# Performance work log

Hardware: AMD Instinct MI355X
Metric: run time of the kernel (lower is better)

The kernel has to match this reference:

```python
import jax, jax.numpy as jnp
import numpy as np

NUM_QUBITS = 12
NUM_LAYERS = 2
STATE_DIM = 2 ** NUM_QUBITS
BATCH = 4096
TWO_PI = 2 * 3.1416  # matches the original initializer constant


def _u3(theta, phi, lam):
    """Single-qubit U3 gate, 2x2 complex64 (matches TF layer exactly)."""
    c = jnp.cos(theta / 2)
    s = jnp.sin(theta / 2)
    z = jnp.zeros_like(phi)
    e_phi = jnp.exp(jax.lax.complex(z, phi))
    e_lam = jnp.exp(jax.lax.complex(z, lam))
    e_pl = jnp.exp(jax.lax.complex(z, phi + lam))
    cc = jax.lax.complex(c, jnp.zeros_like(c))
    sc = jax.lax.complex(s, jnp.zeros_like(s))
    row1 = jnp.stack([cc, -e_lam * sc])
    row2 = jnp.stack([e_phi * sc, e_pl * cc])
    return jnp.stack([row1, row2])  # [2, 2] complex64


def _full_gate(theta_vec, phi_vec, lam_vec):
    """Kronecker product of per-qubit gates -> [2^n, 2^n] complex64."""
    full = _u3(theta_vec[0], phi_vec[0], lam_vec[0])
    for q in range(1, theta_vec.shape[0]):
        full = jnp.kron(full, _u3(theta_vec[q], phi_vec[q], lam_vec[q]))
    return full


def setup_inputs() -> dict:
    key = jax.random.key(0)
    k1, k2, k3, k4 = jax.random.split(key, 4)
    inputs = jax.random.normal(k1, (BATCH, STATE_DIM), dtype=jnp.float32)
    thetas = jax.random.uniform(k2, (NUM_LAYERS, NUM_QUBITS), minval=0.0, maxval=TWO_PI, dtype=jnp.float32)
    phis = jax.random.uniform(k3, (NUM_LAYERS, NUM_QUBITS), minval=0.0, maxval=TWO_PI, dtype=jnp.float32)
    lams = jax.random.uniform(k4, (NUM_LAYERS, NUM_QUBITS), minval=0.0, maxval=TWO_PI, dtype=jnp.float32)
    return {"inputs": inputs, "thetas": thetas, "phis": phis, "lams": lams}


def reference(inputs, thetas, phis, lams):
    # normalize real inputs as complex state, per-sample L2 norm
    state = jax.lax.complex(inputs, jnp.zeros_like(inputs))  # [B, D] complex64
    norm = jnp.linalg.norm(state, axis=1, keepdims=True)      # real, [B, 1]
    state = state / norm
    for l in range(thetas.shape[0]):
        U = _full_gate(thetas[l], phis[l], lams[l])  # [D, D]
        # matvec(U, x) per sample == state @ U^T, batched GEMM replaces tf.map_fn
        state = state @ U.T
    return jnp.real(state * jnp.conj(state))  # probabilities, [B, D] float32
```

## Files before the change

### kernel.cpp

```cpp
#include <hip/hip_runtime.h>
#include <hip/hip_fp16.h>

#define NQ   12
#define DIM  4096
#define NL   2
#define BATCH 4096

typedef float  v2f __attribute__((ext_vector_type(2)));
typedef __fp16 hv2 __attribute__((ext_vector_type(2)));


struct HGate { __half2 m[8]; };

__global__ void build_gates(const float* __restrict__ th,
                            const float* __restrict__ ph,
                            const float* __restrict__ lm,
                            float* __restrict__ gates) {
    int q = threadIdx.x;
    if (q >= NQ) return;
    float g00r = 1.f, g00i = 0.f, g01r = 0.f, g01i = 0.f;
    float g10r = 0.f, g10i = 0.f, g11r = 1.f, g11i = 0.f;
    #pragma unroll
    for (int l = 0; l < NL; ++l) {
        float th2 = 0.5f * th[l * NQ + q];
        float p   = ph[l * NQ + q];
        float la  = lm[l * NQ + q];
        float s, c, sl, cl, sp, cp, spl, cpl;
        sincosf(th2, &s, &c);
        sincosf(la, &sl, &cl);
        sincosf(p, &sp, &cp);
        sincosf(p + la, &spl, &cpl);
        float u00r = c,        u00i = 0.f;
        float u01r = -cl * s,  u01i = -sl * s;
        float u10r = cp * s,   u10i = sp * s;
        float u11r = cpl * c,  u11i = spl * c;
        float n00r = u00r*g00r - u00i*g00i + u01r*g10r - u01i*g10i;
        float n00i = u00r*g00i + u00i*g00r + u01r*g10i + u01i*g10r;
        float n01r = u00r*g01r - u00i*g01i + u01r*g11r - u01i*g11i;
        float n01i = u00r*g01i + u00i*g01r + u01r*g11i + u01i*g11r;
        float n10r = u10r*g00r - u10i*g00i + u11r*g10r - u11i*g10i;
        float n10i = u10r*g00i + u10i*g00r + u11r*g10i + u11i*g10r;
        float n11r = u10r*g01r - u10i*g01i + u11r*g11r - u11i*g11i;
        float n11i = u10r*g01i + u10i*g01r + u11r*g11i + u11i*g11r;
        g00r = n00r; g00i = n00i; g01r = n01r; g01i = n01i;
        g10r = n10r; g10i = n10i; g11r = n11r; g11i = n11i;
    }
    int k = (NQ - 1) - q;
    __half2* o = reinterpret_cast<__half2*>(gates) + (size_t)k * 8;
    o[0] = __floats2half2_rn(g00r,  g00i);
    o[1] = __floats2half2_rn(-g00i, g00i);
    o[2] = __floats2half2_rn(g01r,  g01i);
    o[3] = __floats2half2_rn(-g01i, g01i);
    o[4] = __floats2half2_rn(g10r,  g10i);
    o[5] = __floats2half2_rn(-g10i, g10i);
    o[6] = __floats2half2_rn(g11r,  g11i);
    o[7] = __floats2half2_rn(-g11i, g11i);
}

__device__ __forceinline__ unsigned h2u(__half2 x) {
    union { __half2 h; unsigned u; } c; c.h = x; return c.u;
}
__device__ __forceinline__ __half2 u2h(unsigned x) {
    union { unsigned u; __half2 h; } c; c.u = x; return c.h;
}
__device__ __forceinline__ __half2 rbroad(float x) {
    union { hv2 a; __half2 b; } c;
    c.a = __builtin_amdgcn_cvt_pkrtz(x, x);
    return c.b;
}

__device__ __forceinline__ __half2 cfma(__half2 g1, __half2 g2, __half2 x,
                                        __half2 acc) {
    acc = __hfma2(__low2half2(g1), x, acc);
    acc = __hfma2(g2, __lowhigh2highlow(x), acc);
    return acc;
}

__device__ __forceinline__ void papply(__half2 v[16], int r0, int r1,
                                       const HGate& g) {
    __half2 x0 = v[r0], x1 = v[r1];
    __half2 a = __hmul2(__low2half2(g.m[2]), x1);
    a = __hfma2(g.m[3], __lowhigh2highlow(x1), a);
    a = cfma(g.m[0], g.m[1], x0, a);
    __half2 b = __hmul2(__low2half2(g.m[6]), x1);
    b = __hfma2(g.m[7], __lowhigh2highlow(x1), b);
    b = cfma(g.m[4], g.m[5], x0, b);
    v[r0] = a; v[r1] = b;
}

__device__ __forceinline__ void papply_rbit(__half2 v[16], int rb,
                                            const HGate& g) {
    const int m = 1 << rb;
    #pragma unroll
    for (int h = 0; h < 8; ++h) {
        int low = h & (m - 1);
        int r   = ((h & ~(m - 1)) << 1) | low;
        papply(v, r, r | m, g);
    }
}

#define K1W(r) ( (((r)&1)*33) + ((((r)>>1)&1)*66) + ((((r)>>2)&1)*264) + ((((r)>>3)&1)*512) )
#define K1R(r) (r)
#define K2W(r) ( ((((r)&1))<<2) | (((((r)>>1)&1))<<3) | (((((r)>>2)&1))<<4) | (((((r)>>3)&1))<<8) )
#define K3R(r) ( (((r)&1)*36) + ((((r)>>1)&1)*72) + ((((r)>>2)&1)*1024) + ((((r)>>3)&1)*2048) )

__global__ __launch_bounds__(256, 8)
void qc_sim(const float* __restrict__ in,
            const HGate* __restrict__ gp,
            float* __restrict__ out) {
    __shared__ unsigned st[DIM];
    __shared__ float red[4];

    const int t    = threadIdx.x;
    const int lane = t & 63;
    const int b    = blockIdx.x;

    const float4* __restrict__ x4 =
        reinterpret_cast<const float4*>(in + (size_t)b * DIM);
    float4 lA[4];
    #pragma unroll
    for (int j = 0; j < 4; ++j) lA[j] = x4[j * 256 + t];

    float ss = 0.f;
    #pragma unroll
    for (int j = 0; j < 4; ++j)
        ss += lA[j].x*lA[j].x + lA[j].y*lA[j].y + lA[j].z*lA[j].z + lA[j].w*lA[j].w;
    #pragma unroll
    for (int off = 32; off > 0; off >>= 1)
        ss += __shfl_down(ss, off, 64);
    if (lane == 0) red[t >> 6] = ss;

    const int L0 = lane & 1, L1 = (lane >> 1) & 1, L2 = (lane >> 2) & 1,
              L3 = (lane >> 3) & 1, L4 = (lane >> 4) & 1, L5 = lane >> 5;
    const int w  = t >> 6, w0 = w & 1, w1 = w >> 1;
    const int A1w = L0 | (L1 << 1) | ((L2 ^ L5) << 2) | (L3 << 3) | (L4 << 4)
                  | (L5 << 7) | (w << 10);
    const int A1r = L0 | (L1 << 1) | (L3 << 2) | (L4 << 3) | (L2 << 4)
                  | (L0 << 5) | (L1 << 6) | (L3 << 7) | (L4 << 8) | (L5 << 9)
                  | (w << 10);
    const int A2w = L0 | (L1 << 1) | (L2 << 2) | (L3 << 3) | (L4 << 4)
                  | (L2 << 5) | (L3 << 6) | (L4 << 7) | (L5 << 9) | (w << 10);
    const int A3  = L0 | (L1 << 1) | (L2 << 2) | (L3 << 3) | ((L4 ^ w0) << 4)
                  | (w0 << 7) | (L5 << 8) | (w1 << 9);

    __half2 v[16];

    {
        HGate g0 = gp[0];
        #pragma unroll
        for (int j = 0; j < 4; ++j) {
            __half2 xx0 = rbroad(lA[j].x), xx1 = rbroad(lA[j].y);
            v[4*j]   = __hfma2(g0.m[2], xx1, __hmul2(g0.m[0], xx0));
            v[4*j+1] = __hfma2(g0.m[6], xx1, __hmul2(g0.m[4], xx0));
            xx0 = rbroad(lA[j].z); xx1 = rbroad(lA[j].w);
            v[4*j+2] = __hfma2(g0.m[2], xx1, __hmul2(g0.m[0], xx0));
            v[4*j+3] = __hfma2(g0.m[6], xx1, __hmul2(g0.m[4], xx0));
        }
        { HGate g = gp[1];  papply_rbit(v, 1, g); }
        { HGate g = gp[10]; papply_rbit(v, 2, g); }
        { HGate g = gp[11];
          #pragma unroll
          for (int h = 0; h < 8; ++h) {
              papply(v, h, h | 8, g);
              st[A1w ^ K1W(h)]     = h2u(v[h]);
              st[A1w ^ K1W(h | 8)] = h2u(v[h | 8]);
          }
        }
    }

    #pragma unroll
    for (int r = 0; r < 16; ++r) v[r] = u2h(st[A1r ^ K1R(r)]);

    { HGate g = gp[2]; papply_rbit(v, 0, g); }
    { HGate g = gp[3]; papply_rbit(v, 1, g); }
    { HGate g = gp[4]; papply_rbit(v, 2, g); }
    { HGate g = gp[5];
      #pragma unroll
      for (int h = 0; h < 8; ++h) {
          papply(v, h, h | 8, g);
          st[A2w ^ K2W(h)]     = h2u(v[h]);
          st[A2w ^ K2W(h | 8)] = h2u(v[h | 8]);
      }
    }

    __syncthreads();

    #pragma unroll
    for (int r = 0; r < 16; ++r) v[r] = u2h(st[A3 ^ K3R(r)]);

    { HGate g = gp[6]; papply_rbit(v, 0, g); }
    { HGate g = gp[7]; papply_rbit(v, 1, g); }
    { HGate g = gp[8]; papply_rbit(v, 2, g); }
    { HGate g = gp[9]; papply_rbit(v, 3, g); }

    float inv = 1.0f / (red[0] + red[1] + red[2] + red[3]);
    const int sbase = lane | (w << 10);
    float* __restrict__ o = out + (size_t)b * DIM;
    #pragma unroll
    for (int r = 0; r < 16; ++r) {
        float re = __low2float(v[r]), im = __high2float(v[r]);
        o[sbase + (r << 6)] = (re * re + im * im) * inv;
    }
}

extern "C" void kernel_launch(void* const* d_in, const int* in_sizes, int n_in,
                              void* d_out, int out_size, void* d_ws, size_t ws_size,
                              hipStream_t stream) {
    (void)in_sizes; (void)n_in; (void)out_size; (void)ws_size;
    const float* inputs = (const float*)d_in[0];
    const float* thetas = (const float*)d_in[1];
    const float* phis   = (const float*)d_in[2];
    const float* lams   = (const float*)d_in[3];
    float* gates = (float*)d_ws;
    float* out   = (float*)d_out;

    hipLaunchKernelGGL(build_gates, dim3(1), dim3(64), 0, stream,
                       thetas, phis, lams, gates);
    hipLaunchKernelGGL(qc_sim, dim3(BATCH), dim3(256), 0, stream,
                       inputs, (const HGate*)gates, out);
}
```

Baseline: 128.4 us.

## Process two batch samples per block with packed 64-bit LDS exchanges

Each block now simulates two samples at once. Their half2 amplitudes are packed into 64-bit words for the shared-memory transposes, and the grid is halved. This amortizes gate loads, index math and syncs across two states and uses wider LDS accesses, with new swizzle constants for the 8-byte layout. In exchange it doubles register and LDS use per block, and occupancy is lowered via launch bounds (256,4).

After: 128.1 us. No clear change (-0.2%).

```diff
diff --git a/kernel.cpp b/kernel.cpp
--- a/kernel.cpp
+++ b/kernel.cpp
@@ -69,137 +69,163 @@
     return c.b;
 }
 
-__device__ __forceinline__ __half2 cfma(__half2 g1, __half2 g2, __half2 x,
-                                        __half2 acc) {
-    acc = __hfma2(__low2half2(g1), x, acc);
-    acc = __hfma2(g2, __lowhigh2highlow(x), acc);
-    return acc;
-}
-
-__device__ __forceinline__ void papply(__half2 v[16], int r0, int r1,
-                                       const HGate& g) {
-    __half2 x0 = v[r0], x1 = v[r1];
+__device__ __forceinline__ void cbfly(__half2& x0, __half2& x1, const HGate& g) {
     __half2 a = __hmul2(__low2half2(g.m[2]), x1);
     a = __hfma2(g.m[3], __lowhigh2highlow(x1), a);
-    a = cfma(g.m[0], g.m[1], x0, a);
+    a = __hfma2(__low2half2(g.m[0]), x0, a);
+    a = __hfma2(g.m[1], __lowhigh2highlow(x0), a);
     __half2 b = __hmul2(__low2half2(g.m[6]), x1);
     b = __hfma2(g.m[7], __lowhigh2highlow(x1), b);
-    b = cfma(g.m[4], g.m[5], x0, b);
-    v[r0] = a; v[r1] = b;
-}
-
-__device__ __forceinline__ void papply_rbit(__half2 v[16], int rb,
-                                            const HGate& g) {
+    b = __hfma2(__low2half2(g.m[4]), x0, b);
+    b = __hfma2(g.m[5], __lowhigh2highlow(x0), b);
+    x0 = a; x1 = b;
+}
+
+__device__ __forceinline__ void papplyP(__half2 va[16], __half2 vb[16],
+                                        int r0, int r1, const HGate& g) {
+    cbfly(va[r0], va[r1], g);
+    cbfly(vb[r0], vb[r1], g);
+}
+
+__device__ __forceinline__ void papply_rbitP(__half2 va[16], __half2 vb[16],
+                                             int rb, const HGate& g) {
     const int m = 1 << rb;
     #pragma unroll
     for (int h = 0; h < 8; ++h) {
         int low = h & (m - 1);
         int r   = ((h & ~(m - 1)) << 1) | low;
-        papply(v, r, r | m, g);
-    }
-}
-
-#define K1W(r) ( (((r)&1)*33) + ((((r)>>1)&1)*66) + ((((r)>>2)&1)*264) + ((((r)>>3)&1)*512) )
+        papplyP(va, vb, r, r | m, g);
+    }
+}
+
+__device__ __forceinline__ unsigned long long packP(__half2 a, __half2 b) {
+    return (unsigned long long)h2u(a) | ((unsigned long long)h2u(b) << 32);
+}
+
+#define K1W(r) ( (((r)&1)*17) + ((((r)>>1)&1)*34) + ((((r)>>2)&1)*1024) + ((((r)>>3)&1)*2048) )
 #define K1R(r) (r)
-#define K2W(r) ( ((((r)&1))<<2) | (((((r)>>1)&1))<<3) | (((((r)>>2)&1))<<4) | (((((r)>>3)&1))<<8) )
-#define K3R(r) ( (((r)&1)*36) + ((((r)>>1)&1)*72) + ((((r)>>2)&1)*1024) + ((((r)>>3)&1)*2048) )
-
-__global__ __launch_bounds__(256, 8)
+#define K2W(r) ((r) << 2)
+#define K3R(r) ( (((r)&1)*68) + ((((r)>>1)&1)*136) + ((((r)>>2)&1)*256) + ((((r)>>3)&1)*512) )
+
+__global__ __launch_bounds__(256, 4)
 void qc_sim(const float* __restrict__ in,
             const HGate* __restrict__ gp,
             float* __restrict__ out) {
-    __shared__ unsigned st[DIM];
-    __shared__ float red[4];
+    __shared__ unsigned long long st[DIM];
+    __shared__ float red0[4], red1[4];
 
     const int t    = threadIdx.x;
     const int lane = t & 63;
     const int b    = blockIdx.x;
 
-    const float4* __restrict__ x4 =
-        reinterpret_cast<const float4*>(in + (size_t)b * DIM);
-    float4 lA[4];
-    #pragma unroll
-    for (int j = 0; j < 4; ++j) lA[j] = x4[j * 256 + t];
-
-    float ss = 0.f;
-    #pragma unroll
-    for (int j = 0; j < 4; ++j)
-        ss += lA[j].x*lA[j].x + lA[j].y*lA[j].y + lA[j].z*lA[j].z + lA[j].w*lA[j].w;
-    #pragma unroll
-    for (int off = 32; off > 0; off >>= 1)
-        ss += __shfl_down(ss, off, 64);
-    if (lane == 0) red[t >> 6] = ss;
-
-    const int L0 = lane & 1, L1 = (lane >> 1) & 1, L2 = (lane >> 2) & 1,
-              L3 = (lane >> 3) & 1, L4 = (lane >> 4) & 1, L5 = lane >> 5;
-    const int w  = t >> 6, w0 = w & 1, w1 = w >> 1;
-    const int A1w = L0 | (L1 << 1) | ((L2 ^ L5) << 2) | (L3 << 3) | (L4 << 4)
-                  | (L5 << 7) | (w << 10);
-    const int A1r = L0 | (L1 << 1) | (L3 << 2) | (L4 << 3) | (L2 << 4)
-                  | (L0 << 5) | (L1 << 6) | (L3 << 7) | (L4 << 8) | (L5 << 9)
-                  | (w << 10);
-    const int A2w = L0 | (L1 << 1) | (L2 << 2) | (L3 << 3) | (L4 << 4)
-                  | (L2 << 5) | (L3 << 6) | (L4 << 7) | (L5 << 9) | (w << 10);
-    const int A3  = L0 | (L1 << 1) | (L2 << 2) | (L3 << 3) | ((L4 ^ w0) << 4)
-                  | (w0 << 7) | (L5 << 8) | (w1 << 9);
-
-    __half2 v[16];
+    const float4* __restrict__ x40 =
+        reinterpret_cast<const float4*>(in + (size_t)(2 * b) * DIM);
+    const float4* __restrict__ x41 =
+        reinterpret_cast<const float4*>(in + (size_t)(2 * b + 1) * DIM);
+    float4 lA[4], lB[4];
+    #pragma unroll
+    for (int j = 0; j < 4; ++j) lA[j] = x40[j * 256 + t];
+    #pragma unroll
+    for (int j = 0; j < 4; ++j) lB[j] = x41[j * 256 + t];
+
+    float s0 = 0.f, s1 = 0.f;
+    #pragma unroll
+    for (int j = 0; j < 4; ++j) {
+        s0 += lA[j].x*lA[j].x + lA[j].y*lA[j].y + lA[j].z*lA[j].z + lA[j].w*lA[j].w;
+        s1 += lB[j].x*lB[j].x + lB[j].y*lB[j].y + lB[j].z*lB[j].z + lB[j].w*lB[j].w;
+    }
+    #pragma unroll
+    for (int off = 32; off > 0; off >>= 1) {
+        s0 += __shfl_down(s0, off, 64);
+        s1 += __shfl_down(s1, off, 64);
+    }
+    if (lane == 0) { red0[t >> 6] = s0; red1[t >> 6] = s1; }
+
+    const int T0 = lane & 1, T1 = (lane >> 1) & 1, T2 = (lane >> 2) & 1,
+              T3 = (lane >> 3) & 1, T4 = (lane >> 4) & 1, T5 = lane >> 5;
+    const int w  = t >> 6;
+    const int A1w = T0 | (T1 << 1) | ((T2 ^ T4) << 2) | ((T3 ^ T5) << 3)
+                  | (T4 << 6) | (T5 << 7) | (w << 8);
+    const int A1r = T0 | (T1 << 1) | (T2 << 2) | (T3 << 3)
+                  | (T0 << 4) | (T1 << 5) | (T2 << 6) | (T3 << 7)
+                  | (w << 8) | (T4 << 10) | (T5 << 11);
+    const int A2w = T0 | (T1 << 1) | (T2 << 2) | (T3 << 3)
+                  | (T2 << 6) | (T3 << 7) | (w << 8) | (T4 << 10) | (T5 << 11);
+    const int A3  = lane | (w << 10);
+
+    __half2 va[16], vb[16];
 
     {
         HGate g0 = gp[0];
         #pragma unroll
         for (int j = 0; j < 4; ++j) {
-            __half2 xx0 = rbroad(lA[j].x), xx1 = rbroad(lA[j].y);
-            v[4*j]   = __hfma2(g0.m[2], xx1, __hmul2(g0.m[0], xx0));
-            v[4*j+1] = __hfma2(g0.m[6], xx1, __hmul2(g0.m[4], xx0));
-            xx0 = rbroad(lA[j].z); xx1 = rbroad(lA[j].w);
-            v[4*j+2] = __hfma2(g0.m[2], xx1, __hmul2(g0.m[0], xx0));
-            v[4*j+3] = __hfma2(g0.m[6], xx1, __hmul2(g0.m[4], xx0));
+            __half2 p0 = rbroad(lA[j].x), p1 = rbroad(lA[j].y);
+            va[4*j]   = __hfma2(g0.m[2], p1, __hmul2(g0.m[0], p0));
+            va[4*j+1] = __hfma2(g0.m[6], p1, __hmul2(g0.m[4], p0));
+            p0 = rbroad(lA[j].z); p1 = rbroad(lA[j].w);
+            va[4*j+2] = __hfma2(g0.m[2], p1, __hmul2(g0.m[0], p0));
+            va[4*j+3] = __hfma2(g0.m[6], p1, __hmul2(g0.m[4], p0));
+            p0 = rbroad(lB[j].x); p1 = rbroad(lB[j].y);
+            vb[4*j]   = __hfma2(g0.m[2], p1, __hmul2(g0.m[0], p0));
+            vb[4*j+1] = __hfma2(g0.m[6], p1, __hmul2(g0.m[4], p0));
+            p0 = rbroad(lB[j].z); p1 = rbroad(lB[j].w);
+            vb[4*j+2] = __hfma2(g0.m[2], p1, __hmul2(g0.m[0], p0));
+            vb[4*j+3] = __hfma2(g0.m[6], p1, __hmul2(g0.m[4], p0));
         }
-        { HGate g = gp[1];  papply_rbit(v, 1, g); }
-        { HGate g = gp[10]; papply_rbit(v, 2, g); }
+        { HGate g = gp[1];  papply_rbitP(va, vb, 1, g); }
+        { HGate g = gp[10]; papply_rbitP(va, vb, 2, g); }
         { HGate g = gp[11];
           #pragma unroll
           for (int h = 0; h < 8; ++h) {
-              papply(v, h, h | 8, g);
-              st[A1w ^ K1W(h)]     = h2u(v[h]);
-              st[A1w ^ K1W(h | 8)] = h2u(v[h | 8]);
+              papplyP(va, vb, h, h | 8, g);
+              st[A1w ^ K1W(h)]     = packP(va[h],     vb[h]);
+              st[A1w ^ K1W(h | 8)] = packP(va[h | 8], vb[h | 8]);
           }
         }
     }
 
     #pragma unroll
-    for (int r = 0; r < 16; ++r) v[r] = u2h(st[A1r ^ K1R(r)]);
-
-    { HGate g = gp[2]; papply_rbit(v, 0, g); }
-    { HGate g = gp[3]; papply_rbit(v, 1, g); }
-    { HGate g = gp[4]; papply_rbit(v, 2, g); }
+    for (int r = 0; r < 16; ++r) {
+        unsigned long long u = st[A1r ^ K1R(r)];
+        va[r] = u2h((unsigned)u); vb[r] = u2h((unsigned)(u >> 32));
+    }
+
+    { HGate g = gp[2]; papply_rbitP(va, vb, 0, g); }
+    { HGate g = gp[3]; papply_rbitP(va, vb, 1, g); }
+    { HGate g = gp[4]; papply_rbitP(va, vb, 2, g); }
     { HGate g = gp[5];
       #pragma unroll
       for (int h = 0; h < 8; ++h) {
-          papply(v, h, h | 8, g);
-          st[A2w ^ K2W(h)]     = h2u(v[h]);
-          st[A2w ^ K2W(h | 8)] = h2u(v[h | 8]);
+          papplyP(va, vb, h, h | 8, g);
+          st[A2w ^ K2W(h)]     = packP(va[h],     vb[h]);
+          st[A2w ^ K2W(h | 8)] = packP(va[h | 8], vb[h | 8]);
       }
     }
 
     __syncthreads();
 
     #pragma unroll
-    for (int r = 0; r < 16; ++r) v[r] = u2h(st[A3 ^ K3R(r)]);
-
-    { HGate g = gp[6]; papply_rbit(v, 0, g); }
-    { HGate g = gp[7]; papply_rbit(v, 1, g); }
-    { HGate g = gp[8]; papply_rbit(v, 2, g); }
-    { HGate g = gp[9]; papply_rbit(v, 3, g); }
-
-    float inv = 1.0f / (red[0] + red[1] + red[2] + red[3]);
+    for (int r = 0; r < 16; ++r) {
+        unsigned long long u = st[A3 ^ K3R(r)];
+        va[r] = u2h((unsigned)u); vb[r] = u2h((unsigned)(u >> 32));
+    }
+
+    { HGate g = gp[6]; papply_rbitP(va, vb, 0, g); }
+    { HGate g = gp[7]; papply_rbitP(va, vb, 1, g); }
+    { HGate g = gp[8]; papply_rbitP(va, vb, 2, g); }
+    { HGate g = gp[9]; papply_rbitP(va, vb, 3, g); }
+
+    float inv0 = 1.0f / (red0[0] + red0[1] + red0[2] + red0[3]);
+    float inv1 = 1.0f / (red1[0] + red1[1] + red1[2] + red1[3]);
     const int sbase = lane | (w << 10);
-    float* __restrict__ o = out + (size_t)b * DIM;
+    float* __restrict__ o0 = out + (size_t)(2 * b) * DIM;
+    float* __restrict__ o1 = out + (size_t)(2 * b + 1) * DIM;
     #pragma unroll
     for (int r = 0; r < 16; ++r) {
-        float re = __low2float(v[r]), im = __high2float(v[r]);
-        o[sbase + (r << 6)] = (re * re + im * im) * inv;
+        float re = __low2float(va[r]), im = __high2float(va[r]);
+        o0[sbase + (r << 6)] = (re * re + im * im) * inv0;
+        re = __low2float(vb[r]); im = __high2float(vb[r]);
+        o1[sbase + (r << 6)] = (re * re + im * im) * inv1;
     }
 }
 
@@ -216,6 +242,6 @@
 
     hipLaunchKernelGGL(build_gates, dim3(1), dim3(64), 0, stream,
                        thetas, phis, lams, gates);
-    hipLaunchKernelGGL(qc_sim, dim3(BATCH), dim3(256), 0, stream,
+    hipLaunchKernelGGL(qc_sim, dim3(BATCH / 2), dim3(256), 0, stream,
                        inputs, (const HGate*)gates, out);
 }
```
